# Kernel optimization log

Hardware: AMD Instinct MI355X
Metric: run time of the kernel (lower is better)

## Reference

```python
import jax, jax.numpy as jnp
import numpy as np

# dims matching init_kwargs
B, N = 1, 2048
VOCAB, DIM, DEPTH = 32000, 1024, 4
HEADS, DIM_HEAD, WINDOW = 16, 64, 512
INNER = HEADS * DIM_HEAD          # 1024
FF_INNER = int(DIM * 4 * 2 / 3)   # 2730 (GEGLU inner)
DPB_DIM = DIM // 2
LN_EPS = 1e-5


def layernorm(x, g, b):
    m = jnp.mean(x, axis=-1, keepdims=True)
    v = jnp.mean(jnp.square(x - m), axis=-1, keepdims=True)
    return (x - m) * jax.lax.rsqrt(v + LN_EPS) * g + b


def look_around(x, backward=1, forward=0, pad_value=-1):
    # x: [b, nw, w, ...]; concat shifted windows along the window_size axis
    nw = x.shape[1]
    pads = [(0, 0), (backward, forward)] + [(0, 0)] * (x.ndim - 2)
    px = jnp.pad(x, pads, constant_values=pad_value)
    return jnp.concatenate([px[:, i:i + nw] for i in range(backward + forward + 1)], axis=2)


def dynamic_pos_bias(w1, b1, w2, b2, w3, b3, i, j):
    # MLP over scalar relative distances, then gather into [H, i, j]
    rel = jnp.arange(j, dtype=jnp.float32)[:, None]            # [j, 1]
    h = jax.nn.silu(rel @ w1 + b1)
    h = jax.nn.silu(h @ w2 + b2)
    bias = h @ w3 + b3                                          # [j, H]
    idx = jnp.abs(jnp.arange(j - i, j)[:, None] - jnp.arange(j)[None, :])  # [i, j]
    return jnp.transpose(bias[idx], (2, 0, 1))                  # [H, i, j]


def local_attention(q, k, v, attn_bias):
    # causal sliding-window attention, look_backward=1, look_forward=0, exact_windowsize=True
    # q,k,v: [B,H,N,dh]; N assumed multiple of WINDOW (autopad is a no-op then)
    b, h, n, d = q.shape
    w = WINDOW
    nw = n // w
    scale = d ** -0.5
    bq = q.reshape(b * h, nw, w, d) * scale
    bk = look_around(k.reshape(b * h, nw, w, d), pad_value=-1.0)   # [bh,nw,2w,d]
    bv = look_around(v.reshape(b * h, nw, w, d), pad_value=-1.0)
    t = jnp.arange(n).reshape(1, nw, w)
    bq_t = t[..., :, None]                                      # [1,nw,w,1]
    bq_k = look_around(t, pad_value=-1)[..., None, :]           # [1,nw,1,2w]
    # causal | exact-window | padding masks
    mask = (bq_t < bq_k) | (bq_t > bq_k + w) | (bq_k == -1)
    sim = jnp.einsum('bwid,bwjd->bwij', bq, bk)                 # [bh,nw,w,2w]
    sim = (sim.reshape(b, h, nw, w, 2 * w) + attn_bias[None, :, None]).reshape(b * h, nw, w, 2 * w)
    sim = jnp.where(mask, -jnp.finfo(sim.dtype).max, sim)
    attn = jax.nn.softmax(sim, axis=-1)
    out = jnp.einsum('bwij,bwjd->bwid', attn, bv)
    return out.reshape(b, h, n, d)


def forward(tokens, tok_emb, pos_emb, dpb_w1, dpb_b1, dpb_w2, dpb_b2, dpb_w3, dpb_b3,
            ln1_g, ln1_b, Wqkv, Wo, ln2_g, ln2_b, Wff1, Wff2, lnf_g, lnf_b, Wlogits):
    bsz, n = tokens.shape
    x = tok_emb[tokens] + pos_emb[:n]                           # [B,N,D]
    bias = dynamic_pos_bias(dpb_w1, dpb_b1, dpb_w2, dpb_b2, dpb_w3, dpb_b3, WINDOW, 2 * WINDOW)

    def split_heads(t):
        return t.reshape(bsz, n, HEADS, DIM_HEAD).transpose(0, 2, 1, 3)

    for l in range(DEPTH):
        # LocalMHA (prenorm) + residual
        h = layernorm(x, ln1_g[l], ln1_b[l])
        q, k, v = jnp.split(h @ Wqkv[l], 3, axis=-1)
        o = local_attention(split_heads(q), split_heads(k), split_heads(v), bias)
        o = o.transpose(0, 2, 1, 3).reshape(bsz, n, INNER)
        x = x + o @ Wo[l]
        # GEGLU FFN (prenorm inside FeedForward) + residual
        h = layernorm(x, ln2_g[l], ln2_b[l])
        a, gate = jnp.split(h @ Wff1[l], 2, axis=-1)
        x = x + (a * jax.nn.gelu(gate, approximate=False)) @ Wff2[l]

    return layernorm(x, lnf_g, lnf_b) @ Wlogits                 # [B,N,V]


def setup_inputs() -> dict:
    key = jax.random.key(0)
    ks = iter(jax.random.split(key, 16))
    s = 0.02
    rn = lambda *shape: jax.random.normal(next(ks), shape, dtype=jnp.float32) * s
    return {
        'tokens': jax.random.randint(next(ks), (B, N), 0, VOCAB, dtype=jnp.int32),
        'tok_emb': rn(VOCAB, DIM),
        'pos_emb': rn(N, DIM),
        'dpb_w1': rn(1, DPB_DIM), 'dpb_b1': jnp.zeros((DPB_DIM,), jnp.float32),
        'dpb_w2': rn(DPB_DIM, DPB_DIM), 'dpb_b2': jnp.zeros((DPB_DIM,), jnp.float32),
        'dpb_w3': rn(DPB_DIM, HEADS), 'dpb_b3': jnp.zeros((HEADS,), jnp.float32),
        'ln1_g': jnp.ones((DEPTH, DIM), jnp.float32), 'ln1_b': jnp.zeros((DEPTH, DIM), jnp.float32),
        'Wqkv': rn(DEPTH, DIM, 3 * INNER),
        'Wo': rn(DEPTH, INNER, DIM),
        'ln2_g': jnp.ones((DEPTH, DIM), jnp.float32), 'ln2_b': jnp.zeros((DEPTH, DIM), jnp.float32),
        'Wff1': rn(DEPTH, DIM, 2 * FF_INNER),
        'Wff2': rn(DEPTH, FF_INNER, DIM),
        'lnf_g': jnp.ones((DIM,), jnp.float32), 'lnf_b': jnp.zeros((DIM,), jnp.float32),
        'Wlogits': rn(DIM, VOCAB),
    }


def reference(tokens, tok_emb, pos_emb, dpb_w1, dpb_b1, dpb_w2, dpb_b2, dpb_w3, dpb_b3,
              ln1_g, ln1_b, Wqkv, Wo, ln2_g, ln2_b, Wff1, Wff2, lnf_g, lnf_b, Wlogits):
    return forward(tokens, tok_emb, pos_emb, dpb_w1, dpb_b1, dpb_w2, dpb_b2, dpb_w3, dpb_b3,
                   ln1_g, ln1_b, Wqkv, Wo, ln2_g, ln2_b, Wff1, Wff2, lnf_g, lnf_b, Wlogits)
```

## Files before the change

kernel.cpp:

```cpp
#include <hip/hip_runtime.h>
#include <cstdint>

#define DEV __device__ __forceinline__

typedef __attribute__((ext_vector_type(8))) short bf16x8;
typedef __attribute__((ext_vector_type(4))) short bf16x4;
typedef __attribute__((ext_vector_type(4))) float f32x4;
typedef __attribute__((ext_vector_type(8))) unsigned short u16x8;

DEV float bf2f(unsigned short u) { return __uint_as_float(((unsigned)u) << 16); }
DEV unsigned short f2bf(float f) {
  unsigned u = __float_as_uint(f);
  u += 0x7FFFu + ((u >> 16) & 1u);
  return (unsigned short)(u >> 16);
}

DEV void gload_lds16(const void* g, void* lds) {
  __builtin_amdgcn_global_load_lds(
      (const __attribute__((address_space(1))) unsigned int*)g,
      (__attribute__((address_space(3))) unsigned int*)lds, 16, 0, 0);
}

__global__ __launch_bounds__(256) void k_prep(
    const int* __restrict__ tokens, const float* __restrict__ tok_emb,
    const float* __restrict__ pos_emb, float* __restrict__ x,
    const float* __restrict__ w1, const float* __restrict__ b1,
    const float* __restrict__ w2, const float* __restrict__ b2,
    const float* __restrict__ w3, const float* __restrict__ b3,
    float* __restrict__ table,
    const float* __restrict__ Wqkv, unsigned short* __restrict__ WqkvT,
    const float* __restrict__ Wo, unsigned short* __restrict__ WoT,
    const float* __restrict__ Wff1, unsigned short* __restrict__ Wff1T,
    const float* __restrict__ Wff2, unsigned short* __restrict__ Wff2T,
    const float* __restrict__ Wlog, unsigned short* __restrict__ WlogT) {
  __shared__ unsigned short sm16[8192];
  int b = blockIdx.x, t = threadIdx.x;
  if (b < 2048) {
    int tok = tokens[b];
    int c = t * 4;
    float4 a = *(const float4*)(tok_emb + (long)tok * 1024 + c);
    float4 p = *(const float4*)(pos_emb + (long)b * 1024 + c);
    float4 r;
    r.x = a.x + p.x; r.y = a.y + p.y; r.z = a.z + p.z; r.w = a.w + p.w;
    *(float4*)(x + (long)b * 1024 + c) = r;
    return;
  }
  b -= 2048;
  if (b < 1024) {
    float* h1 = (float*)sm16;
    float* h2 = h1 + 512;
    float rf = (float)b;
    for (int c = t; c < 512; c += 256) {
      float v = rf * w1[c] + b1[c];
      h1[c] = v / (1.0f + __expf(-v));
    }
    __syncthreads();
    for (int c = t; c < 512; c += 256) {
      float acc = b2[c];
      for (int k2 = 0; k2 < 512; ++k2) acc = fmaf(h1[k2], w2[(long)k2 * 512 + c], acc);
      h2[c] = acc / (1.0f + __expf(-acc));
    }
    __syncthreads();
    if (t < 16) {
      float acc = b3[t];
      for (int k2 = 0; k2 < 512; ++k2) acc = fmaf(h2[k2], w3[k2 * 16 + t], acc);
      table[b * 16 + t] = acc;
    }
    return;
  }
  b -= 1024;
  const float* src; unsigned short* dst;
  int N, Kreal, nt, kt, mode;
  if (b < 1536) {
    int z = b / 384, r = b % 384;
    nt = r / 16; kt = r % 16; mode = 0; N = 3072; Kreal = 1024;
    src = Wqkv + (long)z * 1024 * 3072;
    dst = WqkvT + ((long)z * 384 + r) * 8192;
  } else if ((b -= 1536) < 512) {
    int z = b / 128, r = b % 128;
    nt = r / 16; kt = r % 16; mode = 0; N = 1024; Kreal = 1024;
    src = Wo + (long)z * 1024 * 1024;
    dst = WoT + ((long)z * 128 + r) * 8192;
  } else if ((b -= 512) < 2752) {
    int z = b / 688, r = b % 688;
    nt = r / 16; kt = r % 16; mode = 1; N = 5460; Kreal = 1024;
    src = Wff1 + (long)z * 1024 * 5460;
    dst = Wff1T + ((long)z * 688 + r) * 8192;
  } else if ((b -= 2752) < 1376) {
    int z = b / 344, r = b % 344;
    nt = r / 43; kt = r % 43; mode = 0; N = 1024; Kreal = 2730;
    src = Wff2 + (long)z * 2730 * 1024;
    dst = Wff2T + ((long)z * 344 + r) * 8192;
  } else {
    b -= 1376;
    nt = b / 16; kt = b % 16; mode = 0; N = 32000; Kreal = 1024;
    src = Wlog;
    dst = WlogT + (long)b * 8192;
  }
  const int k0 = kt * 64;
  const int q = t & 31;
  const int kc = t >> 5;
  u16x8 pa, pb, pc, pd;
  if (mode == 0) {
    const int nb = nt * 128 + q * 4;
#pragma unroll
    for (int e = 0; e < 8; ++e) {
      int k = k0 + kc * 8 + e;
      float4 v = {0.f, 0.f, 0.f, 0.f};
      if (k < Kreal) v = *(const float4*)(src + (long)k * N + nb);
      pa[e] = f2bf(v.x); pb[e] = f2bf(v.y); pc[e] = f2bf(v.z); pd[e] = f2bf(v.w);
    }
  } else {
    const int f0 = nt * 64 + q * 2;
#pragma unroll
    for (int e = 0; e < 8; ++e) {
      int k = k0 + kc * 8 + e;
      const float* sr = src + (long)k * 5460;
      float2 af = {0.f, 0.f}, gf = {0.f, 0.f};
      if (f0 + 1 < 2730) {
        af = *(const float2*)(sr + f0);
        gf = *(const float2*)(sr + 2730 + f0);
      } else if (f0 < 2730) {
        af.x = sr[f0];
        gf.x = sr[2730 + f0];
      }
      pa[e] = f2bf(af.x); pb[e] = f2bf(gf.x); pc[e] = f2bf(af.y); pd[e] = f2bf(gf.y);
    }
  }
  {
    const int r0 = q * 4;
    *(u16x8*)&sm16[(r0 + 0) * 64 + ((kc ^ ((r0 + 0) & 7)) * 8)] = pa;
    *(u16x8*)&sm16[(r0 + 1) * 64 + ((kc ^ ((r0 + 1) & 7)) * 8)] = pb;
    *(u16x8*)&sm16[(r0 + 2) * 64 + ((kc ^ ((r0 + 2) & 7)) * 8)] = pc;
    *(u16x8*)&sm16[(r0 + 3) * 64 + ((kc ^ ((r0 + 3) & 7)) * 8)] = pd;
  }
  __syncthreads();
#pragma unroll
  for (int i2 = 0; i2 < 4; ++i2)
    *(u16x8*)(dst + i2 * 2048 + t * 8) = *(const u16x8*)&sm16[i2 * 2048 + t * 8];
}

__global__ __launch_bounds__(256) void k_ln4(const float* __restrict__ x,
    const float* __restrict__ g, const float* __restrict__ b,
    unsigned short* __restrict__ out) {
  const int row = blockIdx.x * 4 + (threadIdx.x >> 6);
  const int l = threadIdx.x & 63;
  const float* xr = x + (long)row * 1024 + l * 16;
  float4 v[4];
#pragma unroll
  for (int e = 0; e < 4; ++e) v[e] = ((const float4*)xr)[e];
  float s = 0.0f;
#pragma unroll
  for (int e = 0; e < 4; ++e) s += v[e].x + v[e].y + v[e].z + v[e].w;
#pragma unroll
  for (int off = 32; off; off >>= 1) s += __shfl_xor(s, off);
  float mean = s * (1.0f / 1024.0f);
  float sq = 0.0f;
#pragma unroll
  for (int e = 0; e < 4; ++e) {
    float a0 = v[e].x - mean, a1 = v[e].y - mean, a2 = v[e].z - mean, a3 = v[e].w - mean;
    sq += a0 * a0 + a1 * a1 + a2 * a2 + a3 * a3;
  }
#pragma unroll
  for (int off = 32; off; off >>= 1) sq += __shfl_xor(sq, off);
  float inv = rsqrtf(sq * (1.0f / 1024.0f) + 1e-5f);
  const float* gr = g + l * 16;
  const float* br = b + l * 16;
  unsigned short* orow = out + (long)row * 1024 + l * 16;
#pragma unroll
  for (int e = 0; e < 4; ++e) {
    float4 gv = ((const float4*)gr)[e];
    float4 bv = ((const float4*)br)[e];
    ushort4 o;
    o.x = f2bf((v[e].x - mean) * inv * gv.x + bv.x);
    o.y = f2bf((v[e].y - mean) * inv * gv.y + bv.y);
    o.z = f2bf((v[e].z - mean) * inv * gv.z + bv.z);
    o.w = f2bf((v[e].w - mean) * inv * gv.w + bv.w);
    ((ushort4*)orow)[e] = o;
  }
}

__global__ __launch_bounds__(256, 2) void k_attn_mfma(
    const unsigned short* __restrict__ qkv, const float* __restrict__ table,
    unsigned short* __restrict__ o) {
  __shared__ unsigned short Ks[64 * 64];
  __shared__ unsigned short Vt[64 * 72];
  __shared__ unsigned short Ps[4][16 * 72];
  __shared__ float biasl[1024];
  const int qt = blockIdx.x, h = blockIdx.y, wi = blockIdx.z;
  const int iw0 = qt * 64;
  const int t = threadIdx.x;
  const int w = t >> 6, l = t & 63;
  const int lq = l & 15, lk = l >> 4;

  for (int i = t; i < 1024; i += 256) biasl[i] = table[i * 16 + h];

  const unsigned short* qp = qkv + (long)(wi * 512 + iw0 + w * 16 + lq) * 3072 + h * 64;
  bf16x8 qf0 = *(const bf16x8*)(qp + lk * 8);
  bf16x8 qf1 = *(const bf16x8*)(qp + 32 + lk * 8);

  f32x4 oacc[4] = {};
  float mrun[4] = {-3.0e38f, -3.0e38f, -3.0e38f, -3.0e38f};
  float srun[4] = {};

  const int kt0 = (wi == 0) ? 8 : qt;
  const int kt1 = qt + 8;
  for (int kt = kt0; kt <= kt1; ++kt) {
    const int ktbase = kt * 64;
    const long kgbase = (long)((wi - 1) * 512 + ktbase);
    __syncthreads();
    {
      const unsigned short* Kg = qkv + kgbase * 3072 + 1024 + h * 64;
#pragma unroll
      for (int s2 = 0; s2 < 2; ++s2) {
        int g = s2 * 4 + w;
        int row = g * 8 + (l >> 3);
        int gch = (l & 7) ^ (row & 7);
        gload_lds16(Kg + (long)row * 3072 + gch * 8, &Ks[g * 512]);
      }
    }
    {
      int kp = t & 31, dg = t >> 5;
      const unsigned short* Vg =
          qkv + (kgbase + 2 * kp) * 3072 + 2048 + h * 64 + dg * 8;
      bf16x8 a0 = *(const bf16x8*)Vg;
      bf16x8 a1 = *(const bf16x8*)(Vg + 3072);
#pragma unroll
      for (int e = 0; e < 8; ++e) {
        unsigned pack = ((unsigned)(unsigned short)a0[e]) |
                        (((unsigned)(unsigned short)a1[e]) << 16);
        *(unsigned*)&Vt[(dg * 8 + e) * 72 + 2 * kp] = pack;
      }
    }
    asm volatile("s_waitcnt vmcnt(0)" ::: "memory");
    __syncthreads();

    f32x4 sacc[4] = {};
#pragma unroll
    for (int ct = 0; ct < 4; ++ct) {
      int krow = ct * 16 + lq;
      bf16x8 kf0 = *(const bf16x8*)&Ks[krow * 64 + (((0 + lk) ^ (krow & 7)) * 8)];
      bf16x8 kf1 = *(const bf16x8*)&Ks[krow * 64 + (((4 + lk) ^ (krow & 7)) * 8)];
      sacc[ct] = __builtin_amdgcn_mfma_f32_16x16x32_bf16(qf0, kf0, sacc[ct], 0, 0, 0);
      sacc[ct] = __builtin_amdgcn_mfma_f32_16x16x32_bf16(qf1, kf1, sacc[ct], 0, 0, 0);
    }

#pragma unroll
    for (int r = 0; r < 4; ++r) {
      const int iw = iw0 + w * 16 + lk * 4 + r;
      float sc[4];
#pragma unroll
      for (int ct = 0; ct < 4; ++ct) {
        int jj = ktbase + ct * 16 + lq;
        int di = 512 + iw - jj;
        int dic = min(max(di, 0), 1023);
        bool allowed = (jj >= iw) && (jj <= iw + 512);
        float v = sacc[ct][r] * 0.125f + biasl[dic];
        sc[ct] = allowed ? v : -3.0e38f;
      }
      float mx = fmaxf(fmaxf(sc[0], sc[1]), fmaxf(sc[2], sc[3]));
      mx = fmaxf(mx, __shfl_xor(mx, 1));
      mx = fmaxf(mx, __shfl_xor(mx, 2));
      mx = fmaxf(mx, __shfl_xor(mx, 4));
      mx = fmaxf(mx, __shfl_xor(mx, 8));
      float mnew = fmaxf(mrun[r], mx);
      float f = __expf(mrun[r] - mnew);
      mrun[r] = mnew;
      float rs = 0.0f;
#pragma unroll
      for (int ct = 0; ct < 4; ++ct) {
        float pv = __expf(sc[ct] - mnew);
        rs += pv;
        Ps[w][(lk * 4 + r) * 72 + ct * 16 + lq] = f2bf(pv);
      }
      rs += __shfl_xor(rs, 1);
      rs += __shfl_xor(rs, 2);
      rs += __shfl_xor(rs, 4);
      rs += __shfl_xor(rs, 8);
      srun[r] = srun[r] * f + rs;
#pragma unroll
      for (int dt = 0; dt < 4; ++dt) oacc[dt][r] *= f;
    }
    asm volatile("s_waitcnt lgkmcnt(0)" ::: "memory");

#pragma unroll
    for (int ks = 0; ks < 2; ++ks) {
      bf16x4 pa0 = *(const bf16x4*)&Ps[w][lq * 72 + ks * 32 + lk * 8];
      bf16x4 pa1 = *(const bf16x4*)&Ps[w][lq * 72 + ks * 32 + lk * 8 + 4];
      bf16x8 pa = __builtin_shufflevector(pa0, pa1, 0, 1, 2, 3, 4, 5, 6, 7);
#pragma unroll
      for (int dt = 0; dt < 4; ++dt) {
        int drow = dt * 16 + lq;
        bf16x4 vb0 = *(const bf16x4*)&Vt[drow * 72 + ks * 32 + lk * 8];
        bf16x4 vb1 = *(const bf16x4*)&Vt[drow * 72 + ks * 32 + lk * 8 + 4];
        bf16x8 vb = __builtin_shufflevector(vb0, vb1, 0, 1, 2, 3, 4, 5, 6, 7);
        oacc[dt] = __builtin_amdgcn_mfma_f32_16x16x32_bf16(pa, vb, oacc[dt], 0, 0, 0);
      }
    }
  }

  unsigned short* ob =
      o + (long)(wi * 512 + iw0 + w * 16 + lk * 4) * 1024 + h * 64 + lq;
#pragma unroll
  for (int r = 0; r < 4; ++r) {
    float inv = 1.0f / srun[r];
#pragma unroll
    for (int dt = 0; dt < 4; ++dt)
      ob[(long)r * 1024 + dt * 16] = f2bf(oacc[dt][r] * inv);
  }
}

template <int EPI, int BM>
__global__ __launch_bounds__(256, 2) void k_gemm(const unsigned short* __restrict__ A,
    const unsigned short* __restrict__ BTt, void* __restrict__ Cout,
    int N, int K, int nbm) {
  constexpr int MI = BM / 32;
  __shared__ unsigned short As[BM * 64];
  __shared__ unsigned short Bs[128 * 64];
  const int nwg = gridDim.x;
  const int orig = blockIdx.x;
  const int q8 = nwg >> 3, r8 = nwg & 7;
  const int xcd = orig & 7, i8 = orig >> 3;
  const int wgid = (xcd < r8 ? xcd * (q8 + 1) : r8 * (q8 + 1) + (xcd - r8) * q8) + i8;
  const int bm = wgid % nbm;
  const int bn = wgid / nbm;
  const int t = threadIdx.x;
  const int w = t >> 6, l = t & 63;
  const int wm = w >> 1, wn = w & 1;
  const int lrow = l >> 3, lch = l & 7;
  const int lq = l & 15, lk = l >> 4;
  f32x4 acc[MI][4] = {};
  const long arow0 = (long)bm * BM;
  const unsigned short* btile = BTt + (long)bn * (K >> 6) * 8192;
  for (int kt = 0; kt < K; kt += 64) {
    __syncthreads();
    const unsigned short* bsrc = btile + (long)(kt >> 6) * 8192 + l * 8;
#pragma unroll
    for (int s2 = 0; s2 < 4; ++s2) {
      int grp = s2 * 4 + w;
      gload_lds16(bsrc + grp * 512, &Bs[grp * 512]);
      if (s2 < MI) {
        int r = grp * 8 + lrow;
        int gch = lch ^ lrow;
        gload_lds16(A + (arow0 + r) * K + kt + gch * 8, &As[grp * 512]);
      }
    }
    asm volatile("s_waitcnt vmcnt(0)" ::: "memory");
    __syncthreads();
#pragma unroll
    for (int kk = 0; kk < 2; ++kk) {
      bf16x8 af[MI], bfr[4];
#pragma unroll
      for (int i = 0; i < MI; ++i) {
        int ra = wm * (BM / 2) + i * 16 + lq;
        af[i] = *(const bf16x8*)&As[ra * 64 + (((kk * 4 + lk) ^ (ra & 7)) * 8)];
      }
#pragma unroll
      for (int j = 0; j < 4; ++j) {
        int rb = wn * 64 + j * 16 + lq;
        bfr[j] = *(const bf16x8*)&Bs[rb * 64 + (((kk * 4 + lk) ^ (rb & 7)) * 8)];
      }
#pragma unroll
      for (int i = 0; i < MI; ++i)
#pragma unroll
        for (int j = 0; j < 4; ++j)
          acc[i][j] = __builtin_amdgcn_mfma_f32_16x16x32_bf16(af[i], bfr[j],
                                                              acc[i][j], 0, 0, 0);
    }
  }
  const int rbase = bm * BM + wm * (BM / 2) + lk * 4;
  const int cbase = bn * 128 + wn * 64 + lq;
#pragma unroll
  for (int i = 0; i < MI; ++i) {
#pragma unroll
    for (int j = 0; j < 4; ++j) {
#pragma unroll
      for (int r2 = 0; r2 < 4; ++r2) {
        long row = rbase + i * 16 + r2;
        long col = cbase + j * 16;
        float v = acc[i][j][r2];
        if (EPI == 0) {
          ((unsigned short*)Cout)[row * N + col] = f2bf(v);
        } else if (EPI == 1) {
          ((float*)Cout)[row * N + col] += v;
        } else if (EPI == 2) {
          ((float*)Cout)[row * N + col] = v;
        } else {
          float gpart = __shfl_xor(v, 1);
          if ((lq & 1) == 0) {
            float uval =
                v * (0.5f * gpart * (1.0f + erff(gpart * 0.70710678118654752f)));
            ((unsigned short*)Cout)[row * (N >> 1) + (col >> 1)] = f2bf(uval);
          }
        }
      }
    }
  }
}

extern "C" void kernel_launch(void* const* d_in, const int* in_sizes, int n_in,
                              void* d_out, int out_size, void* d_ws, size_t ws_size,
                              hipStream_t stream) {
  (void)in_sizes; (void)n_in; (void)out_size; (void)ws_size;
  const int* tokens   = (const int*)d_in[0];
  const float* tok_emb = (const float*)d_in[1];
  const float* pos_emb = (const float*)d_in[2];
  const float* dpb_w1 = (const float*)d_in[3];
  const float* dpb_b1 = (const float*)d_in[4];
  const float* dpb_w2 = (const float*)d_in[5];
  const float* dpb_b2 = (const float*)d_in[6];
  const float* dpb_w3 = (const float*)d_in[7];
  const float* dpb_b3 = (const float*)d_in[8];
  const float* ln1_g  = (const float*)d_in[9];
  const float* ln1_b  = (const float*)d_in[10];
  const float* Wqkv   = (const float*)d_in[11];
  const float* Wo     = (const float*)d_in[12];
  const float* ln2_g  = (const float*)d_in[13];
  const float* ln2_b  = (const float*)d_in[14];
  const float* Wff1   = (const float*)d_in[15];
  const float* Wff2   = (const float*)d_in[16];
  const float* lnf_g  = (const float*)d_in[17];
  const float* lnf_b  = (const float*)d_in[18];
  const float* Wlog   = (const float*)d_in[19];
  float* out = (float*)d_out;

  char* p = (char*)d_ws;
  auto carve = [&](size_t bytes) {
    char* q = p;
    p += (bytes + 255) & ~(size_t)255;
    return (void*)q;
  };
  unsigned short* WqkvT = (unsigned short*)carve((size_t)4 * 3072 * 1024 * 2);
  unsigned short* WoT   = (unsigned short*)carve((size_t)4 * 1024 * 1024 * 2);
  unsigned short* Wff1T = (unsigned short*)carve((size_t)4 * 5504 * 1024 * 2);
  unsigned short* Wff2T = (unsigned short*)carve((size_t)4 * 1024 * 2752 * 2);
  unsigned short* WlogT = (unsigned short*)carve((size_t)32000 * 1024 * 2);
  float*          x     = (float*)carve((size_t)2048 * 1024 * 4);
  unsigned short* hbuf  = (unsigned short*)carve((size_t)2048 * 1024 * 2);
  unsigned short* qkv   = (unsigned short*)carve((size_t)2048 * 3072 * 2);
  unsigned short* ao    = (unsigned short*)carve((size_t)2048 * 1024 * 2);
  unsigned short* ubuf  = (unsigned short*)carve((size_t)2048 * 2752 * 2);
  float*          table = (float*)carve((size_t)1024 * 16 * 4);

  k_prep<<<13248, 256, 0, stream>>>(
      tokens, tok_emb, pos_emb, x, dpb_w1, dpb_b1, dpb_w2, dpb_b2, dpb_w3,
      dpb_b3, table, Wqkv, WqkvT, Wo, WoT, Wff1, Wff1T, Wff2, Wff2T, Wlog, WlogT);

  for (int l = 0; l < 4; ++l) {
    k_ln4<<<512, 256, 0, stream>>>(x, ln1_g + l * 1024, ln1_b + l * 1024, hbuf);
    k_gemm<0, 128><<<dim3(16 * (3072 / 128)), 256, 0, stream>>>(
        hbuf, WqkvT + (long)l * 3072 * 1024, qkv, 3072, 1024, 16);
    k_attn_mfma<<<dim3(8, 16, 4), 256, 0, stream>>>(qkv, table, ao);
    k_gemm<1, 64><<<dim3(32 * (1024 / 128)), 256, 0, stream>>>(
        ao, WoT + (long)l * 1024 * 1024, x, 1024, 1024, 32);
    k_ln4<<<512, 256, 0, stream>>>(x, ln2_g + l * 1024, ln2_b + l * 1024, hbuf);
    k_gemm<3, 128><<<dim3(16 * (5504 / 128)), 256, 0, stream>>>(
        hbuf, Wff1T + (long)l * 5504 * 1024, ubuf, 5504, 1024, 16);
    k_gemm<1, 64><<<dim3(32 * (1024 / 128)), 256, 0, stream>>>(
        ubuf, Wff2T + (long)l * 1024 * 2752, x, 1024, 2752, 32);
  }
  k_ln4<<<512, 256, 0, stream>>>(x, lnf_g, lnf_b, hbuf);
  k_gemm<2, 128><<<dim3(16 * (32000 / 128)), 256, 0, stream>>>(
      hbuf, WlogT, out, 32000, 1024, 16);
}
```

Measured before the change: 1.048 ms.

## Double-buffer GEMM LDS tiles and transpose position-bias table for coalesced loads

The GEMM kernel now keeps two LDS buffers for the A and B tiles. It issues the global-to-LDS loads for the next K tile before computing MFMAs on the current one, so memory latency overlaps with compute. One barrier per iteration remains, after the wait. Separately, the position-bias table is stored head-major, so each attention block loads its head's bias with a single coalesced float4 per thread instead of strided scalar reads. Double buffering doubles GEMM LDS use (up to 64KB for BM=128), which may reduce occupancy below the launch-bounds target of two blocks per CU.

```diff
diff --git a/kernel.cpp b/kernel.cpp
--- a/kernel.cpp
+++ b/kernel.cpp
@@ -27,7 +27,7 @@
     const float* __restrict__ w1, const float* __restrict__ b1,
     const float* __restrict__ w2, const float* __restrict__ b2,
     const float* __restrict__ w3, const float* __restrict__ b3,
-    float* __restrict__ table,
+    float* __restrict__ tableT,
     const float* __restrict__ Wqkv, unsigned short* __restrict__ WqkvT,
     const float* __restrict__ Wo, unsigned short* __restrict__ WoT,
     const float* __restrict__ Wff1, unsigned short* __restrict__ Wff1T,
@@ -64,7 +64,7 @@
     if (t < 16) {
       float acc = b3[t];
       for (int k2 = 0; k2 < 512; ++k2) acc = fmaf(h2[k2], w3[k2 * 16 + t], acc);
-      table[b * 16 + t] = acc;
+      tableT[t * 1024 + b] = acc;
     }
     return;
   }
@@ -181,7 +181,7 @@
 }
 
 __global__ __launch_bounds__(256, 2) void k_attn_mfma(
-    const unsigned short* __restrict__ qkv, const float* __restrict__ table,
+    const unsigned short* __restrict__ qkv, const float* __restrict__ tableT,
     unsigned short* __restrict__ o) {
   __shared__ unsigned short Ks[64 * 64];
   __shared__ unsigned short Vt[64 * 72];
@@ -193,7 +193,7 @@
   const int w = t >> 6, l = t & 63;
   const int lq = l & 15, lk = l >> 4;
 
-  for (int i = t; i < 1024; i += 256) biasl[i] = table[i * 16 + h];
+  *(float4*)&biasl[t * 4] = *(const float4*)(tableT + h * 1024 + t * 4);
 
   const unsigned short* qp = qkv + (long)(wi * 512 + iw0 + w * 16 + lq) * 3072 + h * 64;
   bf16x8 qf0 = *(const bf16x8*)(qp + lk * 8);
@@ -315,8 +315,8 @@
     const unsigned short* __restrict__ BTt, void* __restrict__ Cout,
     int N, int K, int nbm) {
   constexpr int MI = BM / 32;
-  __shared__ unsigned short As[BM * 64];
-  __shared__ unsigned short Bs[128 * 64];
+  __shared__ unsigned short As[2][BM * 64];
+  __shared__ unsigned short Bs[2][128 * 64];
   const int nwg = gridDim.x;
   const int orig = blockIdx.x;
   const int q8 = nwg >> 3, r8 = nwg & 7;
@@ -331,34 +331,41 @@
   const int lq = l & 15, lk = l >> 4;
   f32x4 acc[MI][4] = {};
   const long arow0 = (long)bm * BM;
-  const unsigned short* btile = BTt + (long)bn * (K >> 6) * 8192;
-  for (int kt = 0; kt < K; kt += 64) {
-    __syncthreads();
-    const unsigned short* bsrc = btile + (long)(kt >> 6) * 8192 + l * 8;
+  const int NT = K >> 6;
+  const unsigned short* btile = BTt + (long)bn * NT * 8192;
+
+  auto STAGE = [&](int buf, int kt) {
+    const unsigned short* bsrc = btile + (long)kt * 8192 + l * 8;
 #pragma unroll
     for (int s2 = 0; s2 < 4; ++s2) {
       int grp = s2 * 4 + w;
-      gload_lds16(bsrc + grp * 512, &Bs[grp * 512]);
+      gload_lds16(bsrc + grp * 512, &Bs[buf][grp * 512]);
       if (s2 < MI) {
         int r = grp * 8 + lrow;
         int gch = lch ^ lrow;
-        gload_lds16(A + (arow0 + r) * K + kt + gch * 8, &As[grp * 512]);
-      }
-    }
-    asm volatile("s_waitcnt vmcnt(0)" ::: "memory");
-    __syncthreads();
+        gload_lds16(A + (arow0 + r) * K + kt * 64 + gch * 8, &As[buf][grp * 512]);
+      }
+    }
+  };
+
+  STAGE(0, 0);
+  asm volatile("s_waitcnt vmcnt(0)" ::: "memory");
+  __syncthreads();
+  for (int kt = 0; kt < NT; ++kt) {
+    const int cur = kt & 1;
+    if (kt + 1 < NT) STAGE(cur ^ 1, kt + 1);
 #pragma unroll
     for (int kk = 0; kk < 2; ++kk) {
       bf16x8 af[MI], bfr[4];
 #pragma unroll
       for (int i = 0; i < MI; ++i) {
         int ra = wm * (BM / 2) + i * 16 + lq;
-        af[i] = *(const bf16x8*)&As[ra * 64 + (((kk * 4 + lk) ^ (ra & 7)) * 8)];
+        af[i] = *(const bf16x8*)&As[cur][ra * 64 + (((kk * 4 + lk) ^ (ra & 7)) * 8)];
       }
 #pragma unroll
       for (int j = 0; j < 4; ++j) {
         int rb = wn * 64 + j * 16 + lq;
-        bfr[j] = *(const bf16x8*)&Bs[rb * 64 + (((kk * 4 + lk) ^ (rb & 7)) * 8)];
+        bfr[j] = *(const bf16x8*)&Bs[cur][rb * 64 + (((kk * 4 + lk) ^ (rb & 7)) * 8)];
       }
 #pragma unroll
       for (int i = 0; i < MI; ++i)
@@ -367,6 +374,8 @@
           acc[i][j] = __builtin_amdgcn_mfma_f32_16x16x32_bf16(af[i], bfr[j],
                                                               acc[i][j], 0, 0, 0);
     }
+    asm volatile("s_waitcnt vmcnt(0)" ::: "memory");
+    __syncthreads();
   }
   const int rbase = bm * BM + wm * (BM / 2) + lk * 4;
   const int cbase = bn * 128 + wn * 64 + lq;
@@ -440,17 +449,17 @@
   unsigned short* qkv   = (unsigned short*)carve((size_t)2048 * 3072 * 2);
   unsigned short* ao    = (unsigned short*)carve((size_t)2048 * 1024 * 2);
   unsigned short* ubuf  = (unsigned short*)carve((size_t)2048 * 2752 * 2);
-  float*          table = (float*)carve((size_t)1024 * 16 * 4);
+  float*          tableT = (float*)carve((size_t)16 * 1024 * 4);
 
   k_prep<<<13248, 256, 0, stream>>>(
       tokens, tok_emb, pos_emb, x, dpb_w1, dpb_b1, dpb_w2, dpb_b2, dpb_w3,
-      dpb_b3, table, Wqkv, WqkvT, Wo, WoT, Wff1, Wff1T, Wff2, Wff2T, Wlog, WlogT);
+      dpb_b3, tableT, Wqkv, WqkvT, Wo, WoT, Wff1, Wff1T, Wff2, Wff2T, Wlog, WlogT);
 
   for (int l = 0; l < 4; ++l) {
     k_ln4<<<512, 256, 0, stream>>>(x, ln1_g + l * 1024, ln1_b + l * 1024, hbuf);
     k_gemm<0, 128><<<dim3(16 * (3072 / 128)), 256, 0, stream>>>(
         hbuf, WqkvT + (long)l * 3072 * 1024, qkv, 3072, 1024, 16);
-    k_attn_mfma<<<dim3(8, 16, 4), 256, 0, stream>>>(qkv, table, ao);
+    k_attn_mfma<<<dim3(8, 16, 4), 256, 0, stream>>>(qkv, tableT, ao);
     k_gemm<1, 64><<<dim3(32 * (1024 / 128)), 256, 0, stream>>>(
         ao, WoT + (long)l * 1024 * 1024, x, 1024, 1024, 32);
     k_ln4<<<512, 256, 0, stream>>>(x, ln2_g + l * 1024, ln2_b + l * 1024, hbuf);
```

After: 1.168 ms. +11.5%, slower.
